# Performance work log

Hardware: AMD Instinct MI355X
Metric: run time of the kernel (lower is better)

The kernel has to match this reference:

```python
import jax, jax.numpy as jnp
import numpy as np

B, N, H, E = 32, 8192, 128, 10

def setup_inputs() -> dict:
    key = jax.random.key(0)
    ks = jax.random.split(key, 16)
    nrm = lambda k, s: jax.random.normal(k, s, dtype=jnp.float32) * 0.05
    z = lambda s: jnp.zeros(s, dtype=jnp.float32)
    o = lambda s: jnp.ones(s, dtype=jnp.float32)
    return {
        'points': jax.random.normal(ks[0], (B, N, 3), dtype=jnp.float32),
        'category_ids': jax.random.randint(ks[1], (B,), 0, E, dtype=jnp.int32),
        'pr_w1': nrm(ks[2], (3, H)), 'pr_b1': z((H,)), 'pr_g1': o((H,)), 'pr_be1': z((H,)),
        'pr_w2': nrm(ks[3], (H, H)), 'pr_b2': z((H,)), 'pr_g2': o((H,)), 'pr_be2': z((H,)),
        'cat_emb': nrm(ks[4], (E, H)),
        'cr_w1': nrm(ks[5], (2 * H, H)), 'cr_b1': z((H,)), 'cr_g1': o((H,)), 'cr_be1': z((H,)),
        'cr_w2': nrm(ks[6], (H, H // 2)), 'cr_b2': z((H // 2,)), 'cr_g2': o((H // 2,)), 'cr_be2': z((H // 2,)),
        'cr_w3': nrm(ks[7], (H // 2, 3)), 'cr_b3': z((3,)),
        'sy_w1': nrm(ks[8], (3, H // 2)), 'sy_b1': z((H // 2,)), 'sy_g1': o((H // 2,)), 'sy_be1': z((H // 2,)),
        'sy_w2': nrm(ks[9], (H // 2, 3)), 'sy_b2': z((3,)),
        'sp_w1': nrm(ks[10], (E, 3, H)), 'sp_b1': z((E, H)), 'sp_g1': o((E, H)), 'sp_be1': z((E, H)),
        'sp_w2': nrm(ks[11], (E, H, H // 2)), 'sp_b2': z((E, H // 2)), 'sp_g2': o((E, H // 2)), 'sp_be2': z((E, H // 2)),
        'sp_w3': nrm(ks[12], (E, H // 2, 3)), 'sp_b3': z((E, 3)),
    }

def _ln(x, g, b):
    mu = jnp.mean(x, -1, keepdims=True)
    var = jnp.mean((x - mu) ** 2, -1, keepdims=True)
    return (x - mu) * jax.lax.rsqrt(var + 1e-5) * g + b

def _lrelu(x):
    return jnp.where(x >= 0, x, 0.2 * x)

def reference(points, category_ids,
              pr_w1, pr_b1, pr_g1, pr_be1, pr_w2, pr_b2, pr_g2, pr_be2,
              cat_emb,
              cr_w1, cr_b1, cr_g1, cr_be1, cr_w2, cr_b2, cr_g2, cr_be2, cr_w3, cr_b3,
              sy_w1, sy_b1, sy_g1, sy_be1, sy_w2, sy_b2,
              sp_w1, sp_b1, sp_g1, sp_be1, sp_w2, sp_b2, sp_g2, sp_be2, sp_w3, sp_b3):
    xyz = points[..., :3]
    # shared point refinement MLP
    pf = _lrelu(_ln(points @ pr_w1 + pr_b1, pr_g1, pr_be1))
    pf = _lrelu(_ln(pf @ pr_w2 + pr_b2, pr_g2, pr_be2))  # [B,N,H]
    ce = cat_emb[category_ids][:, None, :]  # [B,1,H]
    comb = jnp.concatenate([pf, jnp.broadcast_to(ce, pf.shape)], axis=-1)  # [B,N,2H]
    h = _lrelu(_ln(comb @ cr_w1 + cr_b1, cr_g1, cr_be1))
    h = _lrelu(_ln(h @ cr_w2 + cr_b2, cr_g2, cr_be2))
    offsets = h @ cr_w3 + cr_b3  # [B,N,3]
    # category-conditioned expert MLPs (MoE dispatch via per-sample gather)
    g = lambda p: p[category_ids]
    ph = jnp.einsum('bni,bio->bno', xyz, g(sp_w1)) + g(sp_b1)[:, None, :]
    ph = _lrelu(_ln(ph, g(sp_g1)[:, None, :], g(sp_be1)[:, None, :]))
    ph = jnp.einsum('bni,bio->bno', ph, g(sp_w2)) + g(sp_b2)[:, None, :]
    ph = _lrelu(_ln(ph, g(sp_g2)[:, None, :], g(sp_be2)[:, None, :]))
    prior = jnp.einsum('bni,bio->bno', ph, g(sp_w3)) + g(sp_b3)[:, None, :]
    offsets = offsets + 0.5 * prior
    # symmetry refinement for categories 2 and 8 (mirror x)
    flip = jnp.array([-1.0, 1.0, 1.0], dtype=points.dtype)
    mx = xyz * flip
    s = _lrelu(_ln(mx @ sy_w1 + sy_b1, sy_g1, sy_be1))
    s = (s @ sy_w2 + sy_b2) * flip
    mask = ((category_ids == 2) | (category_ids == 8))[:, None, None]
    offsets = jnp.where(mask, (offsets + s) * 0.5, offsets)
    return offsets
```

## Files before the change

### kernel.cpp

```cpp
#include <hip/hip_runtime.h>
#include <hip/hip_bf16.h>
#include <stdint.h>

typedef __attribute__((ext_vector_type(8))) short bf16x8;
typedef __attribute__((ext_vector_type(4))) float f32x4;

#define NT 256

#define WS_CE    0
#define WS_PR1   16384
#define WS_PR2   24576
#define WS_CR1   57344
#define WS_CR2   90112
#define WS_CR3   106496
#define WS_SY1   108544
#define WS_SY2   112640
#define WS_SP1   114688
#define WS_SP2   196608
#define WS_SP3   360448


__device__ __forceinline__ short bf1(float x) {
    unsigned u = __float_as_uint(x);
    return (short)((u + 0x7fffu + ((u >> 16) & 1u)) >> 16);
}
__device__ __forceinline__ float bfval(short h) {
    return __uint_as_float(((unsigned)(unsigned short)h) << 16);
}
__device__ __forceinline__ unsigned cvtpk(float lo, float hi) {
    unsigned r;
    asm("v_cvt_pk_bf16_f32 %0, %1, %2" : "=v"(r) : "v"(lo), "v"(hi));
    return r;
}

template<int CTRL>
__device__ __forceinline__ float dpp_add(float v) {
    int o = __builtin_amdgcn_mov_dpp(__float_as_int(v), CTRL, 0xf, 0xf, true);
    return v + __int_as_float(o);
}
__device__ __forceinline__ float row16_sum(float v) {
    v = dpp_add<0x128>(v);
    v = dpp_add<0x124>(v);
    v = dpp_add<0x122>(v);
    v = dpp_add<0x121>(v);
    return v;
}

template<int NF>
__device__ __forceinline__ void init_acc(f32x4* acc, const float* __restrict__ bias, int c) {
#pragma unroll
    for (int f = 0; f < NF; ++f) {
        const float bv = bias[f * 16 + c];
        acc[f]     = (f32x4){bv, bv, bv, bv};
        acc[8 + f] = (f32x4){bv, bv, bv, bv};
    }
}
__device__ __forceinline__ void init_b3(f32x4& a0, f32x4& a1, const float* __restrict__ b3, int c) {
    const float bv = (c < 3) ? b3[c] : 0.f;
    a0 = (f32x4){bv, bv, bv, bv};
    a1 = (f32x4){bv, bv, bv, bv};
}

__device__ __forceinline__ bf16x8 mkA6(float a0, float a1, float a2, bool active) {
    bf16x8 A = (bf16x8){0, 0, 0, 0, 0, 0, 0, 0};
    if (active) {
        const short h0 = bf1(a0), h1 = bf1(a1), h2 = bf1(a2);
        A[0] = h0; A[1] = h1; A[2] = h2;
        A[3] = bf1(a0 - bfval(h0));
        A[4] = bf1(a1 - bfval(h1));
        A[5] = bf1(a2 - bfval(h2));
    }
    return A;
}

template<int NF>
__device__ __forceinline__ void mfma_reg(bf16x8 A0, bf16x8 A1, const char* __restrict__ Bg,
                                         int lane, f32x4* acc) {
#pragma unroll
    for (int f = 0; f < NF; ++f) {
        bf16x8 B = *(const bf16x8*)(Bg + f * 1024 + lane * 16);
        acc[f]     = __builtin_amdgcn_mfma_f32_16x16x32_bf16(A0, B, acc[f], 0, 0, 0);
        acc[8 + f] = __builtin_amdgcn_mfma_f32_16x16x32_bf16(A1, B, acc[8 + f], 0, 0, 0);
    }
}

template<int NF, int KS>
__device__ __forceinline__ void mfma_lds(const char* actb, const char* __restrict__ Bg,
                                         int R0c, int g, int lane, f32x4* acc) {
    const int swz = (R0c & 7) << 4;
#pragma unroll
    for (int ks = 0; ks < KS; ++ks) {
        const int kb = ks * 64 + g * 16;
        bf16x8 A0 = *(const bf16x8*)(actb + ((R0c * 256 + kb) ^ swz));
        bf16x8 A1 = *(const bf16x8*)(actb + (((R0c + 16) * 256 + kb) ^ swz));
#pragma unroll
        for (int f = 0; f < NF; ++f) {
            bf16x8 B = *(const bf16x8*)(Bg + (f * KS + ks) * 1024 + lane * 16);
            acc[f]     = __builtin_amdgcn_mfma_f32_16x16x32_bf16(A0, B, acc[f], 0, 0, 0);
            acc[8 + f] = __builtin_amdgcn_mfma_f32_16x16x32_bf16(A1, B, acc[8 + f], 0, 0, 0);
        }
    }
}

__device__ __forceinline__ void mfma3(const char* actb, const char* __restrict__ Bg,
                                      int R0c, int g, int lane, f32x4& a0, f32x4& a1) {
    const int swz = (R0c & 7) << 4;
#pragma unroll
    for (int ks = 0; ks < 2; ++ks) {
        const int kb = ks * 64 + g * 16;
        bf16x8 A0 = *(const bf16x8*)(actb + ((R0c * 256 + kb) ^ swz));
        bf16x8 A1 = *(const bf16x8*)(actb + (((R0c + 16) * 256 + kb) ^ swz));
        bf16x8 B = *(const bf16x8*)(Bg + ks * 1024 + lane * 16);
        a0 = __builtin_amdgcn_mfma_f32_16x16x32_bf16(A0, B, a0, 0, 0, 0);
        a1 = __builtin_amdgcn_mfma_f32_16x16x32_bf16(A1, B, a1, 0, 0, 0);
    }
}

template<int NF>
__device__ __forceinline__ void ln_lrelu_frag(f32x4* acc, int c,
                                              const float* __restrict__ g,
                                              const float* __restrict__ be, float invN) {
    float gv[NF], bev[NF];
#pragma unroll
    for (int f = 0; f < NF; ++f) { gv[f] = g[f * 16 + c]; bev[f] = be[f * 16 + c]; }
#pragma unroll
    for (int rf = 0; rf < 2; ++rf) {
        f32x4 s1 = acc[rf * 8];
        f32x4 s2 = acc[rf * 8] * acc[rf * 8];
#pragma unroll
        for (int f = 1; f < NF; ++f) {
            s1 += acc[rf * 8 + f];
            s2 += acc[rf * 8 + f] * acc[rf * 8 + f];
        }
#pragma unroll
        for (int q = 0; q < 4; ++q) { s1[q] = row16_sum(s1[q]); s2[q] = row16_sum(s2[q]); }
        const f32x4 mu = s1 * invN;
        f32x4 ri;
#pragma unroll
        for (int q = 0; q < 4; ++q)
            ri[q] = rsqrtf(fmaf(s2[q], invN, -mu[q] * mu[q]) + 1e-5f);
#pragma unroll
        for (int f = 0; f < NF; ++f) {
            f32x4 x = (acc[rf * 8 + f] - mu) * ri;
            x = x * gv[f] + bev[f];
            acc[rf * 8 + f] = __builtin_elementwise_max(x, 0.2f * x);
        }
    }
}

template<int NF>
__device__ __forceinline__ void pack_store(char* dst, f32x4* acc, int R0, int c, int g) {
#pragma unroll
    for (int rf = 0; rf < 2; ++rf)
#pragma unroll
        for (int q = 0; q < 4; ++q) {
            const int row = R0 + rf * 16 + g * 4 + q;
            const int rbase = row * 256;
            const int swz = (row & 7) << 4;
#pragma unroll
            for (int m = 0; m < NF / 2; ++m) {
                const unsigned val = cvtpk(acc[rf * 8 + m][q], acc[rf * 8 + m + NF / 2][q]);
                *(unsigned*)(dst + ((rbase + (m * 16 + c) * 4) ^ swz)) = val;
            }
        }
}


__global__ void ce_precompute_kernel(const int* __restrict__ cats,
                                     const float* __restrict__ cat_emb,
                                     const float* __restrict__ cr_w1,
                                     const float* __restrict__ cr_b1,
                                     float* __restrict__ ce_out) {
    const int bb = blockIdx.x;
    const int j = threadIdx.x;
    const int c = cats[bb];
    float acc = cr_b1[j];
#pragma unroll 4
    for (int k = 0; k < 128; ++k)
        acc = fmaf(cat_emb[c * 128 + k], cr_w1[(128 + k) * 128 + j], acc);
    ce_out[bb * 128 + j] = acc;
}

__global__ void wfrag_kernel(
    const float* __restrict__ pr_w1, const float* __restrict__ pr_w2,
    const float* __restrict__ cr_w1, const float* __restrict__ cr_w2,
    const float* __restrict__ cr_w3, const float* __restrict__ sy_w1,
    const float* __restrict__ sy_w2, const float* __restrict__ sp_w1,
    const float* __restrict__ sp_w2, const float* __restrict__ sp_w3,
    char* __restrict__ ws)
{
    const int id = blockIdx.x * 256 + threadIdx.x;
    int local, KS, base, cat = 0;
    const float* W = nullptr;
    int mode;
    int Nstride = 0;

    if (id < 512)        { local = id;          KS = 1; base = WS_PR1; W = pr_w1; mode = 0; Nstride = 128; }
    else if (id < 2560)  { local = id - 512;    KS = 4; base = WS_PR2; W = pr_w2; mode = 1; Nstride = 128; }
    else if (id < 4608)  { local = id - 2560;   KS = 4; base = WS_CR1; W = cr_w1; mode = 1; Nstride = 128; }
    else if (id < 5632)  { local = id - 4608;   KS = 4; base = WS_CR2; W = cr_w2; mode = 1; Nstride = 64; }
    else if (id < 5760)  { local = id - 5632;   KS = 2; base = WS_CR3; W = cr_w3; mode = 2; }
    else if (id < 6016)  { local = id - 5760;   KS = 1; base = WS_SY1; W = sy_w1; mode = 0; Nstride = 64; }
    else if (id < 6144)  { local = id - 6016;   KS = 2; base = WS_SY2; W = sy_w2; mode = 2; }
    else if (id < 11264) { int r = id - 6144;  cat = r / 512;  local = r % 512;
                           KS = 1; base = WS_SP1 + cat * 8192;  W = sp_w1 + cat * 384;  mode = 0; Nstride = 128; }
    else if (id < 21504) { int r = id - 11264; cat = r / 1024; local = r % 1024;
                           KS = 4; base = WS_SP2 + cat * 16384; W = sp_w2 + cat * 8192; mode = 1; Nstride = 64; }
    else                 { int r = id - 21504; cat = r / 128;  local = r % 128;
                           KS = 2; base = WS_SP3 + cat * 2048;  W = sp_w3 + cat * 192;  mode = 2; }

    const int lane = local & 63;
    const int fk = local >> 6;
    const int ks = fk % KS;
    const int f = fk / KS;
    const int c = lane & 15;
    const int g = lane >> 4;
    const int n = f * 16 + c;
    const int p0 = ks * 32 + g * 8;

    bf16x8 H;
#pragma unroll
    for (int e = 0; e < 8; ++e) {
        const int p = p0 + e;
        float v = 0.f;
        if (mode == 0)      { if (p < 6) v = W[(p < 3 ? p : p - 3) * Nstride + n]; }
        else if (mode == 1) { const int k = (p >> 1) + (p & 1) * 64; v = W[k * Nstride + n]; }
        else                { const int k = (p >> 1) + (p & 1) * 32; if (n < 3) v = W[k * 3 + n]; }
        H[e] = bf1(v);
    }
    *(bf16x8*)(ws + base + local * 16) = H;
}


__global__ __launch_bounds__(NT, 3)
void shape_refine_mfma6(
    const float* __restrict__ points, const int* __restrict__ cats,
    const float* __restrict__ pr_b1, const float* __restrict__ pr_g1, const float* __restrict__ pr_be1,
    const float* __restrict__ pr_b2, const float* __restrict__ pr_g2, const float* __restrict__ pr_be2,
    const float* __restrict__ cr_g1, const float* __restrict__ cr_be1,
    const float* __restrict__ cr_b2, const float* __restrict__ cr_g2, const float* __restrict__ cr_be2,
    const float* __restrict__ cr_b3,
    const float* __restrict__ sy_b1, const float* __restrict__ sy_g1, const float* __restrict__ sy_be1,
    const float* __restrict__ sy_b2,
    const float* __restrict__ sp_b1, const float* __restrict__ sp_g1, const float* __restrict__ sp_be1,
    const float* __restrict__ sp_b2, const float* __restrict__ sp_g2, const float* __restrict__ sp_be2,
    const float* __restrict__ sp_b3,
    const char* __restrict__ ws,
    float* __restrict__ out)
{
    __shared__ char act[32768];

    const int t = threadIdx.x;
    const int lane = t & 63;
    const int wid = t >> 6;
    const int c = lane & 15;
    const int g = lane >> 4;
    const int R0 = wid * 32;
    const int R0c = R0 + c;

    const int bid = blockIdx.x;
    const int batch = bid >> 6;
    const int pbase = batch * 8192 + (bid & 63) * 128;

    const int cat = __builtin_amdgcn_readfirstlane(cats[batch]);
    const bool sym = (cat == 2) || (cat == 8);

    const float* p0 = points + 3 * (pbase + R0c);
    const float x0 = p0[0], x1 = p0[1], x2 = p0[2];
    const float y0 = p0[48], y1 = p0[49], y2 = p0[50];

    const bf16x8 A0 = mkA6(x0, x1, x2, g == 0);
    const bf16x8 A1 = mkA6(y0, y1, y2, g == 0);

    f32x4 acc[16];
    f32x4 ocr0, ocr1, oo0, oo1;

    init_acc<8>(acc, pr_b1, c);
    mfma_reg<8>(A0, A1, ws + WS_PR1, lane, acc);
    ln_lrelu_frag<8>(acc, c, pr_g1, pr_be1, 1.f / 128.f);
    pack_store<8>(act, acc, R0, c, g);

    init_acc<8>(acc, pr_b2, c);
    mfma_lds<8, 4>(act, ws + WS_PR2, R0c, g, lane, acc);
    ln_lrelu_frag<8>(acc, c, pr_g2, pr_be2, 1.f / 128.f);
    pack_store<8>(act, acc, R0, c, g);

    init_acc<8>(acc, (const float*)(ws + WS_CE) + batch * 128, c);
    mfma_lds<8, 4>(act, ws + WS_CR1, R0c, g, lane, acc);
    ln_lrelu_frag<8>(acc, c, cr_g1, cr_be1, 1.f / 128.f);
    pack_store<8>(act, acc, R0, c, g);

    init_acc<4>(acc, cr_b2, c);
    mfma_lds<4, 4>(act, ws + WS_CR2, R0c, g, lane, acc);
    ln_lrelu_frag<4>(acc, c, cr_g2, cr_be2, 1.f / 64.f);
    pack_store<4>(act, acc, R0, c, g);

    init_b3(ocr0, ocr1, cr_b3, c);
    mfma3(act, ws + WS_CR3, R0c, g, lane, ocr0, ocr1);

    init_acc<8>(acc, sp_b1 + cat * 128, c);
    mfma_reg<8>(A0, A1, ws + WS_SP1 + cat * 8192, lane, acc);
    ln_lrelu_frag<8>(acc, c, sp_g1 + cat * 128, sp_be1 + cat * 128, 1.f / 128.f);
    pack_store<8>(act, acc, R0, c, g);

    init_acc<4>(acc, sp_b2 + cat * 64, c);
    mfma_lds<4, 4>(act, ws + WS_SP2 + cat * 16384, R0c, g, lane, acc);
    ln_lrelu_frag<4>(acc, c, sp_g2 + cat * 64, sp_be2 + cat * 64, 1.f / 64.f);
    pack_store<4>(act, acc, R0, c, g);

    init_b3(oo0, oo1, sp_b3 + cat * 3, c);
    mfma3(act, ws + WS_SP3 + cat * 2048, R0c, g, lane, oo0, oo1);
    oo0 = ocr0 + 0.5f * oo0;
    oo1 = ocr1 + 0.5f * oo1;

    if (sym) {
        init_acc<4>(acc, sy_b1, c);
        const bf16x8 S0 = mkA6(-x0, x1, x2, g == 0);
        const bf16x8 S1 = mkA6(-y0, y1, y2, g == 0);
        mfma_reg<4>(S0, S1, ws + WS_SY1, lane, acc);
        ln_lrelu_frag<4>(acc, c, sy_g1, sy_be1, 1.f / 64.f);
        pack_store<4>(act, acc, R0, c, g);
        f32x4 s0, s1;
        init_b3(s0, s1, sy_b2, c);
        mfma3(act, ws + WS_SY2, R0c, g, lane, s0, s1);
        const float flip = (c == 0) ? -1.f : 1.f;
#pragma unroll
        for (int q = 0; q < 4; ++q) {
            oo0[q] = (oo0[q] + flip * s0[q]) * 0.5f;
            oo1[q] = (oo1[q] + flip * s1[q]) * 0.5f;
        }
    }

    if (c < 3) {
#pragma unroll
        for (int q = 0; q < 4; ++q) {
            const int row0 = R0 + g * 4 + q;
            out[3 * (pbase + row0) + c] = oo0[q];
            out[3 * (pbase + row0 + 16) + c] = oo1[q];
        }
    }
}


extern "C" void kernel_launch(void* const* d_in, const int* in_sizes, int n_in,
                              void* d_out, int out_size, void* d_ws, size_t ws_size,
                              hipStream_t stream) {
    const float* points  = (const float*)d_in[0];
    const int*   cats    = (const int*)  d_in[1];
    const float* pr_w1   = (const float*)d_in[2];
    const float* pr_b1   = (const float*)d_in[3];
    const float* pr_g1   = (const float*)d_in[4];
    const float* pr_be1  = (const float*)d_in[5];
    const float* pr_w2   = (const float*)d_in[6];
    const float* pr_b2   = (const float*)d_in[7];
    const float* pr_g2   = (const float*)d_in[8];
    const float* pr_be2  = (const float*)d_in[9];
    const float* cat_emb = (const float*)d_in[10];
    const float* cr_w1   = (const float*)d_in[11];
    const float* cr_b1   = (const float*)d_in[12];
    const float* cr_g1   = (const float*)d_in[13];
    const float* cr_be1  = (const float*)d_in[14];
    const float* cr_w2   = (const float*)d_in[15];
    const float* cr_b2   = (const float*)d_in[16];
    const float* cr_g2   = (const float*)d_in[17];
    const float* cr_be2  = (const float*)d_in[18];
    const float* cr_w3   = (const float*)d_in[19];
    const float* cr_b3   = (const float*)d_in[20];
    const float* sy_w1   = (const float*)d_in[21];
    const float* sy_b1   = (const float*)d_in[22];
    const float* sy_g1   = (const float*)d_in[23];
    const float* sy_be1  = (const float*)d_in[24];
    const float* sy_w2   = (const float*)d_in[25];
    const float* sy_b2   = (const float*)d_in[26];
    const float* sp_w1   = (const float*)d_in[27];
    const float* sp_b1   = (const float*)d_in[28];
    const float* sp_g1   = (const float*)d_in[29];
    const float* sp_be1  = (const float*)d_in[30];
    const float* sp_w2   = (const float*)d_in[31];
    const float* sp_b2   = (const float*)d_in[32];
    const float* sp_g2   = (const float*)d_in[33];
    const float* sp_be2  = (const float*)d_in[34];
    const float* sp_w3   = (const float*)d_in[35];
    const float* sp_b3   = (const float*)d_in[36];

    char* ws = (char*)d_ws;
    float* out = (float*)d_out;

    ce_precompute_kernel<<<dim3(32), dim3(128), 0, stream>>>(cats, cat_emb, cr_w1, cr_b1, (float*)ws);
    wfrag_kernel<<<dim3(89), dim3(256), 0, stream>>>(pr_w1, pr_w2, cr_w1, cr_w2, cr_w3,
                                                     sy_w1, sy_w2, sp_w1, sp_w2, sp_w3, ws);

    shape_refine_mfma6<<<dim3(2048), dim3(NT), 0, stream>>>(
        points, cats,
        pr_b1, pr_g1, pr_be1,
        pr_b2, pr_g2, pr_be2,
        cr_g1, cr_be1,
        cr_b2, cr_g2, cr_be2,
        cr_b3,
        sy_b1, sy_g1, sy_be1, sy_b2,
        sp_b1, sp_g1, sp_be1,
        sp_b2, sp_g2, sp_be2,
        sp_b3,
        ws, out);
}
```

Baseline: 96.28 us.

## Stage weight fragments into LDS with double-buffered async global-to-LDS loads

Weight fragments for the K=128 layers were read straight from global memory by every wave. They are now copied cooperatively into a double-buffered LDS area with global_load_lds, one k-slice at a time, so the next slice streams in while the current one feeds MFMA. The weight-fragment layout is reordered to f-fastest within each k-slice so every slice is a contiguous chunk. This adds 16KB of LDS per block, which may reduce occupancy, and adds block-wide barriers per k-step.

```diff
diff --git a/kernel.cpp b/kernel.cpp
--- a/kernel.cpp
+++ b/kernel.cpp
@@ -46,6 +46,17 @@
     return v;
 }
 
+template<int BYTES>
+__device__ __forceinline__ void stage(const char* __restrict__ gsrc, char* ldsdst, int t) {
+    const int wu = (t >> 6) << 10;
+#pragma unroll
+    for (int i = 0; i < BYTES / 4096; ++i)
+        __builtin_amdgcn_global_load_lds(
+            (const __attribute__((address_space(1))) void*)(gsrc + i * 4096 + t * 16),
+            (__attribute__((address_space(3))) void*)(ldsdst + i * 4096 + wu),
+            16, 0, 0);
+}
+
 template<int NF>
 __device__ __forceinline__ void init_acc(f32x4* acc, const float* __restrict__ bias, int c) {
 #pragma unroll
@@ -85,20 +96,28 @@
 }
 
 template<int NF, int KS>
-__device__ __forceinline__ void mfma_lds(const char* actb, const char* __restrict__ Bg,
-                                         int R0c, int g, int lane, f32x4* acc) {
+__device__ __forceinline__ void mfma_staged(const char* actb, char* wb,
+                                            const char* __restrict__ Bg,
+                                            int R0c, int g, int lane, int t, f32x4* acc) {
+    constexpr int CH = NF * 1024;
     const int swz = (R0c & 7) << 4;
+    stage<CH>(Bg, wb, t);
+    __syncthreads();
 #pragma unroll
     for (int ks = 0; ks < KS; ++ks) {
+        if (ks + 1 < KS)
+            stage<CH>(Bg + (ks + 1) * CH, wb + ((ks + 1) & 1) * 8192, t);
+        const char* cur = wb + (ks & 1) * 8192;
         const int kb = ks * 64 + g * 16;
         bf16x8 A0 = *(const bf16x8*)(actb + ((R0c * 256 + kb) ^ swz));
         bf16x8 A1 = *(const bf16x8*)(actb + (((R0c + 16) * 256 + kb) ^ swz));
 #pragma unroll
         for (int f = 0; f < NF; ++f) {
-            bf16x8 B = *(const bf16x8*)(Bg + (f * KS + ks) * 1024 + lane * 16);
+            bf16x8 B = *(const bf16x8*)(cur + f * 1024 + lane * 16);
             acc[f]     = __builtin_amdgcn_mfma_f32_16x16x32_bf16(A0, B, acc[f], 0, 0, 0);
             acc[8 + f] = __builtin_amdgcn_mfma_f32_16x16x32_bf16(A1, B, acc[8 + f], 0, 0, 0);
         }
+        __syncthreads();
     }
 }
 
@@ -190,29 +209,29 @@
     char* __restrict__ ws)
 {
     const int id = blockIdx.x * 256 + threadIdx.x;
-    int local, KS, base, cat = 0;
+    int local, NF, base, cat = 0;
     const float* W = nullptr;
     int mode;
     int Nstride = 0;
 
-    if (id < 512)        { local = id;          KS = 1; base = WS_PR1; W = pr_w1; mode = 0; Nstride = 128; }
-    else if (id < 2560)  { local = id - 512;    KS = 4; base = WS_PR2; W = pr_w2; mode = 1; Nstride = 128; }
-    else if (id < 4608)  { local = id - 2560;   KS = 4; base = WS_CR1; W = cr_w1; mode = 1; Nstride = 128; }
-    else if (id < 5632)  { local = id - 4608;   KS = 4; base = WS_CR2; W = cr_w2; mode = 1; Nstride = 64; }
-    else if (id < 5760)  { local = id - 5632;   KS = 2; base = WS_CR3; W = cr_w3; mode = 2; }
-    else if (id < 6016)  { local = id - 5760;   KS = 1; base = WS_SY1; W = sy_w1; mode = 0; Nstride = 64; }
-    else if (id < 6144)  { local = id - 6016;   KS = 2; base = WS_SY2; W = sy_w2; mode = 2; }
+    if (id < 512)        { local = id;          NF = 8; base = WS_PR1; W = pr_w1; mode = 0; Nstride = 128; }
+    else if (id < 2560)  { local = id - 512;    NF = 8; base = WS_PR2; W = pr_w2; mode = 1; Nstride = 128; }
+    else if (id < 4608)  { local = id - 2560;   NF = 8; base = WS_CR1; W = cr_w1; mode = 1; Nstride = 128; }
+    else if (id < 5632)  { local = id - 4608;   NF = 4; base = WS_CR2; W = cr_w2; mode = 1; Nstride = 64; }
+    else if (id < 5760)  { local = id - 5632;   NF = 1; base = WS_CR3; W = cr_w3; mode = 2; }
+    else if (id < 6016)  { local = id - 5760;   NF = 4; base = WS_SY1; W = sy_w1; mode = 0; Nstride = 64; }
+    else if (id < 6144)  { local = id - 6016;   NF = 1; base = WS_SY2; W = sy_w2; mode = 2; }
     else if (id < 11264) { int r = id - 6144;  cat = r / 512;  local = r % 512;
-                           KS = 1; base = WS_SP1 + cat * 8192;  W = sp_w1 + cat * 384;  mode = 0; Nstride = 128; }
+                           NF = 8; base = WS_SP1 + cat * 8192;  W = sp_w1 + cat * 384;  mode = 0; Nstride = 128; }
     else if (id < 21504) { int r = id - 11264; cat = r / 1024; local = r % 1024;
-                           KS = 4; base = WS_SP2 + cat * 16384; W = sp_w2 + cat * 8192; mode = 1; Nstride = 64; }
+                           NF = 4; base = WS_SP2 + cat * 16384; W = sp_w2 + cat * 8192; mode = 1; Nstride = 64; }
     else                 { int r = id - 21504; cat = r / 128;  local = r % 128;
-                           KS = 2; base = WS_SP3 + cat * 2048;  W = sp_w3 + cat * 192;  mode = 2; }
+                           NF = 1; base = WS_SP3 + cat * 2048;  W = sp_w3 + cat * 192;  mode = 2; }
 
     const int lane = local & 63;
     const int fk = local >> 6;
-    const int ks = fk % KS;
-    const int f = fk / KS;
+    const int f = fk % NF;
+    const int ks = fk / NF;
     const int c = lane & 15;
     const int g = lane >> 4;
     const int n = f * 16 + c;
@@ -233,7 +252,7 @@
 
 
 __global__ __launch_bounds__(NT, 3)
-void shape_refine_mfma6(
+void shape_refine_mfma11(
     const float* __restrict__ points, const int* __restrict__ cats,
     const float* __restrict__ pr_b1, const float* __restrict__ pr_g1, const float* __restrict__ pr_be1,
     const float* __restrict__ pr_b2, const float* __restrict__ pr_g2, const float* __restrict__ pr_be2,
@@ -249,6 +268,7 @@
     float* __restrict__ out)
 {
     __shared__ char act[32768];
+    __shared__ char wb[16384];
 
     const int t = threadIdx.x;
     const int lane = t & 63;
@@ -281,17 +301,17 @@
     pack_store<8>(act, acc, R0, c, g);
 
     init_acc<8>(acc, pr_b2, c);
-    mfma_lds<8, 4>(act, ws + WS_PR2, R0c, g, lane, acc);
+    mfma_staged<8, 4>(act, wb, ws + WS_PR2, R0c, g, lane, t, acc);
     ln_lrelu_frag<8>(acc, c, pr_g2, pr_be2, 1.f / 128.f);
     pack_store<8>(act, acc, R0, c, g);
 
     init_acc<8>(acc, (const float*)(ws + WS_CE) + batch * 128, c);
-    mfma_lds<8, 4>(act, ws + WS_CR1, R0c, g, lane, acc);
+    mfma_staged<8, 4>(act, wb, ws + WS_CR1, R0c, g, lane, t, acc);
     ln_lrelu_frag<8>(acc, c, cr_g1, cr_be1, 1.f / 128.f);
     pack_store<8>(act, acc, R0, c, g);
 
     init_acc<4>(acc, cr_b2, c);
-    mfma_lds<4, 4>(act, ws + WS_CR2, R0c, g, lane, acc);
+    mfma_staged<4, 4>(act, wb, ws + WS_CR2, R0c, g, lane, t, acc);
     ln_lrelu_frag<4>(acc, c, cr_g2, cr_be2, 1.f / 64.f);
     pack_store<4>(act, acc, R0, c, g);
 
@@ -304,7 +324,7 @@
     pack_store<8>(act, acc, R0, c, g);
 
     init_acc<4>(acc, sp_b2 + cat * 64, c);
-    mfma_lds<4, 4>(act, ws + WS_SP2 + cat * 16384, R0c, g, lane, acc);
+    mfma_staged<4, 4>(act, wb, ws + WS_SP2 + cat * 16384, R0c, g, lane, t, acc);
     ln_lrelu_frag<4>(acc, c, sp_g2 + cat * 64, sp_be2 + cat * 64, 1.f / 64.f);
     pack_store<4>(act, acc, R0, c, g);
 
@@ -390,7 +410,7 @@
     wfrag_kernel<<<dim3(89), dim3(256), 0, stream>>>(pr_w1, pr_w2, cr_w1, cr_w2, cr_w3,
                                                      sy_w1, sy_w2, sp_w1, sp_w2, sp_w3, ws);
 
-    shape_refine_mfma6<<<dim3(2048), dim3(NT), 0, stream>>>(
+    shape_refine_mfma11<<<dim3(2048), dim3(NT), 0, stream>>>(
         points, cats,
         pr_b1, pr_g1, pr_be1,
         pr_b2, pr_g2, pr_be2,
```

After: 81.18 us. 15.7% less time.
